# Optimization experiments

Measured on AMD Instinct MI355X. Metric: run time of the kernel, lower is better.

Reference implementation:

```python
import jax, jax.numpy as jnp
import numpy as np

B, T, C, H = 8, 1024, 1024, 16
D = C // H  # head dim = 64

def setup_inputs() -> dict:
    key = jax.random.key(0)
    k1, k2, k3 = jax.random.split(key, 3)
    x = jax.random.normal(k1, (B, T, C), dtype=jnp.float32)
    W_attn = jax.random.normal(k2, (C, 3 * C), dtype=jnp.float32) * (1.0 / np.sqrt(C))
    W_proj = jax.random.normal(k3, (C, C), dtype=jnp.float32) * (1.0 / np.sqrt(C))
    # Llama RoPE frequencies: base^(-2i/D)
    omega = (10000.0 ** (-jnp.arange(0, D, 2, dtype=jnp.float32) / D))  # [D/2]
    return {"x": x, "W_attn": W_attn, "W_proj": W_proj, "omega": omega}

def _apply_rope(x, omega):
    # x: [B, T, H, D]; omega: [D/2]
    t = x.shape[1]
    ang = jnp.arange(t, dtype=x.dtype)[:, None] * omega[None, :]  # [T, D/2]
    cos = jnp.cos(ang)[None, :, None, :]  # [1, T, 1, D/2]
    sin = jnp.sin(ang)[None, :, None, :]
    d2 = x.shape[-1] // 2
    x1, x2 = x[..., :d2], x[..., d2:]
    return jnp.concatenate([x1 * cos - x2 * sin, x2 * cos + x1 * sin], axis=-1)

def reference(x, W_attn, W_proj, omega):
    b, t, c = x.shape
    qkv = jnp.einsum('btc,cd->btd', x, W_attn)  # fused QKV projection
    q, k, v = jnp.split(qkv, 3, axis=-1)
    q = q.reshape(b, t, H, D)
    k = k.reshape(b, t, H, D)
    v = v.reshape(b, t, H, D)
    q = _apply_rope(q, omega)
    k = _apply_rope(k, omega)
    # non-causal SDPA
    scale = 1.0 / jnp.sqrt(jnp.asarray(D, dtype=x.dtype))
    scores = jnp.einsum('bqhd,bkhd->bhqk', q, k) * scale
    probs = jax.nn.softmax(scores, axis=-1)
    y = jnp.einsum('bhqk,bkhd->bqhd', probs, v).reshape(b, t, c)
    return jnp.einsum('btc,cd->btd', y, W_proj)
```

## Files before the change

### kernel.cpp

```cpp
#include <hip/hip_runtime.h>
#include <hip/hip_bf16.h>
#include <stdint.h>


typedef __attribute__((ext_vector_type(8))) short short8;
typedef __attribute__((ext_vector_type(4))) float floatx4;
typedef __attribute__((ext_vector_type(2))) unsigned int uint2v;

#define DEV static __device__ __forceinline__

#if __has_builtin(__builtin_amdgcn_exp2f)
#define EXP2(x) __builtin_amdgcn_exp2f(x)
#else
#define EXP2(x) exp2f(x)
#endif

DEV uint16_t f2bf(float f) {
  union { float f; uint32_t i; } v; v.f = f;
  uint32_t u = v.i;
  return (uint16_t)((u + 0x7fffu + ((u >> 16) & 1u)) >> 16);
}

DEV uint32_t pkbf(float a, float b) {
  __hip_bfloat162 h = __float22bfloat162_rn(make_float2(a, b));
  union { __hip_bfloat162 h; uint32_t u; } v; v.h = h;
  return v.u;
}

DEV void async_load16(const uint16_t* g, uint16_t* l) {
  __builtin_amdgcn_global_load_lds(
      (const __attribute__((address_space(1))) void*)g,
      (__attribute__((address_space(3))) void*)l, 16, 0, 0);
}

__global__ __launch_bounds__(256) void prep(
    const float* __restrict__ x, const float* __restrict__ W_attn,
    const float* __restrict__ W_proj, const float* __restrict__ omega,
    uint16_t* __restrict__ xb, uint16_t* __restrict__ Wt_attn,
    uint16_t* __restrict__ Wt_proj, float2* __restrict__ tab) {
  __shared__ uint16_t tile[64][65];
  const int blk = blockIdx.x, tid = threadIdx.x;
  if (blk < 4096) {
    const size_t base = ((size_t)blk * 256 + tid) * 8;
    floatx4 a = *(const floatx4*)(x + base);
    floatx4 b = *(const floatx4*)(x + base + 4);
    short8 s;
    s[0] = (short)f2bf(a[0]); s[1] = (short)f2bf(a[1]);
    s[2] = (short)f2bf(a[2]); s[3] = (short)f2bf(a[3]);
    s[4] = (short)f2bf(b[0]); s[5] = (short)f2bf(b[1]);
    s[6] = (short)f2bf(b[2]); s[7] = (short)f2bf(b[3]);
    *(short8*)(xb + base) = s;
  } else if (blk < 5120) {
    const float* in;
    uint16_t* out;
    int R = 1024, Ccols, bx, by;
    if (blk < 4864) {
      const int idx = blk - 4096;
      in = W_attn; out = Wt_attn; Ccols = 3072;
      bx = idx % 48; by = idx / 48;
    } else {
      const int idx = blk - 4864;
      in = W_proj; out = Wt_proj; Ccols = 1024;
      bx = idx % 16; by = idx / 16;
    }
    const int tx = tid & 63, ty = tid >> 6;
    const int c0 = bx * 64, r0 = by * 64;
    #pragma unroll
    for (int i = 0; i < 64; i += 4)
      tile[ty + i][tx] = f2bf(in[(size_t)(r0 + ty + i) * Ccols + c0 + tx]);
    __syncthreads();
    #pragma unroll
    for (int i = 0; i < 64; i += 4)
      out[(size_t)(c0 + ty + i) * R + r0 + tx] = tile[tx][ty + i];
  } else {
    const int idx = (blk - 5120) * 256 + tid;
    const int t = idx >> 5, d = idx & 31;
    float s, c;
    sincosf((float)t * omega[d], &s, &c);
    tab[idx] = make_float2(c, s);
  }
}

DEV void gemm_core8(const uint16_t* __restrict__ Ag,
                    const uint16_t* __restrict__ Bg,
                    int row0, int col0,
                    uint16_t* As, uint16_t* Bs, floatx4 (&acc)[4][4]) {
  const int tid = threadIdx.x;
  const int wave = tid >> 6, lane = tid & 63;
  const int l15 = lane & 15, quad = lane >> 4;
  const int wrow = wave >> 1, wcol = wave & 1;
  const int sw = l15 & 7;
  const int K = 1024;

  size_t aoff[4], boff[2];
  #pragma unroll
  for (int i = 0; i < 4; i++) {
    const int e = i * 512 + tid;
    const int r = e >> 3, c = e & 7, j = c ^ (r & 7);
    aoff[i] = (size_t)(row0 + r) * K + j * 8;
  }
  #pragma unroll
  for (int i = 0; i < 2; i++) {
    const int e = i * 512 + tid;
    const int r = e >> 3, c = e & 7, j = c ^ (r & 7);
    boff[i] = (size_t)(col0 + r) * K + j * 8;
  }

  #pragma unroll
  for (int t = 0; t < 2; t++) {
    #pragma unroll
    for (int i = 0; i < 2; i++)
      async_load16(Bg + boff[i] + (size_t)t * 64, Bs + t * 8192 + (i * 512 + tid) * 8);
    #pragma unroll
    for (int i = 0; i < 4; i++)
      async_load16(Ag + aoff[i] + (size_t)t * 64, As + t * 16384 + (i * 512 + tid) * 8);
  }

  const floatx4 z4 = {0.f, 0.f, 0.f, 0.f};
  #pragma unroll
  for (int mi = 0; mi < 4; mi++)
    #pragma unroll
    for (int ni = 0; ni < 4; ni++) acc[mi][ni] = z4;

  asm volatile("s_waitcnt vmcnt(6)" ::: "memory");
  __builtin_amdgcn_s_barrier();

  int qa = 0, q2 = 2;
  const int arow = wrow * 64 + l15;
  const int brow = wcol * 64 + l15;
  for (int kt = 0; kt < 16; ++kt) {
    const uint16_t* Aq = As + qa * 16384;
    const uint16_t* Bq = Bs + qa * 8192;
    uint16_t* As2 = As + q2 * 16384;
    uint16_t* Bs2 = Bs + q2 * 8192;
    const size_t k2 = (size_t)(kt + 2) * 64;

    short8 af[4], bfr[4];
    #pragma unroll
    for (int mi = 0; mi < 4; mi++)
      af[mi] = *(const short8*)(Aq + (arow + mi * 16) * 64 + ((quad ^ sw) * 8));
    #pragma unroll
    for (int ni = 0; ni < 4; ni++)
      bfr[ni] = *(const short8*)(Bq + (brow + ni * 16) * 64 + ((quad ^ sw) * 8));
    if (kt < 14) {
      #pragma unroll
      for (int i = 0; i < 2; i++)
        async_load16(Bg + boff[i] + k2, Bs2 + (i * 512 + tid) * 8);
      #pragma unroll
      for (int i = 0; i < 2; i++)
        async_load16(Ag + aoff[i] + k2, As2 + (i * 512 + tid) * 8);
    }
    __builtin_amdgcn_s_barrier();
    asm volatile("s_waitcnt lgkmcnt(0)" ::: "memory");
    __builtin_amdgcn_s_setprio(1);
    #pragma unroll
    for (int mi = 0; mi < 4; mi++)
      #pragma unroll
      for (int ni = 0; ni < 4; ni++)
        acc[mi][ni] = __builtin_amdgcn_mfma_f32_16x16x32_bf16(
            af[mi], bfr[ni], acc[mi][ni], 0, 0, 0);
    __builtin_amdgcn_s_setprio(0);
    __builtin_amdgcn_s_barrier();

    #pragma unroll
    for (int mi = 0; mi < 4; mi++)
      af[mi] = *(const short8*)(Aq + (arow + mi * 16) * 64 + (((4 + quad) ^ sw) * 8));
    #pragma unroll
    for (int ni = 0; ni < 4; ni++)
      bfr[ni] = *(const short8*)(Bq + (brow + ni * 16) * 64 + (((4 + quad) ^ sw) * 8));
    if (kt < 14) {
      #pragma unroll
      for (int i = 2; i < 4; i++)
        async_load16(Ag + aoff[i] + k2, As2 + (i * 512 + tid) * 8);
      asm volatile("s_waitcnt vmcnt(6)" ::: "memory");
    } else if (kt == 14) {
      asm volatile("s_waitcnt vmcnt(0)" ::: "memory");
    }
    __builtin_amdgcn_s_barrier();
    asm volatile("s_waitcnt lgkmcnt(0)" ::: "memory");
    __builtin_amdgcn_s_setprio(1);
    #pragma unroll
    for (int mi = 0; mi < 4; mi++)
      #pragma unroll
      for (int ni = 0; ni < 4; ni++)
        acc[mi][ni] = __builtin_amdgcn_mfma_f32_16x16x32_bf16(
            af[mi], bfr[ni], acc[mi][ni], 0, 0, 0);
    __builtin_amdgcn_s_setprio(0);
    __builtin_amdgcn_s_barrier();

    qa = (qa == 2) ? 0 : qa + 1;
    q2 = (q2 == 2) ? 0 : q2 + 1;
  }
}

__global__ __launch_bounds__(512) void gemm_qkv(
    const uint16_t* __restrict__ A, const uint16_t* __restrict__ Bt,
    const float2* __restrict__ tab,
    uint16_t* __restrict__ Qr, uint16_t* __restrict__ Kr, uint16_t* __restrict__ Vt) {
  __shared__ __align__(16) uint16_t As[3 * 256 * 64];
  __shared__ __align__(16) uint16_t Bs[3 * 128 * 64];
  const int row0 = blockIdx.y * 256, col0 = blockIdx.x * 128;
  floatx4 acc[4][4];
  gemm_core8(A, Bt, row0, col0, As, Bs, acc);

  const int tid = threadIdx.x;
  const int wave = tid >> 6, lane = tid & 63;
  const int l15 = lane & 15, quad = lane >> 4;
  const int cblk = col0 + (wave & 1) * 64;
  const int region = cblk >> 10;
  const int h = (cblk & 1023) >> 6;
  const int rr = row0 + (wave >> 1) * 64;
  const int b = rr >> 10;
  const int tbase = rr & 1023;
  const size_t bh = (size_t)b * 16 + h;

  if (region < 2) {
    uint16_t* dst = (region == 0) ? Qr : Kr;
    const float scl = (region == 0) ? 0.125f * 1.44269504088896f : 1.0f;
    #pragma unroll
    for (int mi = 0; mi < 4; mi++)
      #pragma unroll
      for (int r = 0; r < 4; r++) {
        const int t = tbase + mi * 16 + quad * 4 + r;
        const size_t base = (bh * 1024 + t) * 64;
        const float2 cs0 = tab[t * 32 + l15];
        const float2 cs1 = tab[t * 32 + l15 + 16];
        {
          float x1 = acc[mi][0][r], x2 = acc[mi][2][r];
          dst[base + l15]      = f2bf((x1 * cs0.x - x2 * cs0.y) * scl);
          dst[base + l15 + 32] = f2bf((x2 * cs0.x + x1 * cs0.y) * scl);
        }
        {
          float x1 = acc[mi][1][r], x2 = acc[mi][3][r];
          dst[base + 16 + l15]      = f2bf((x1 * cs1.x - x2 * cs1.y) * scl);
          dst[base + 16 + l15 + 32] = f2bf((x2 * cs1.x + x1 * cs1.y) * scl);
        }
      }
  } else {
    #pragma unroll
    for (int mi = 0; mi < 4; mi++)
      #pragma unroll
      for (int ni = 0; ni < 4; ni++) {
        const int d = ni * 16 + l15;
        #pragma unroll
        for (int r = 0; r < 4; r++) {
          const int t = tbase + mi * 16 + quad * 4 + r;
          Vt[bh * 65536 + (size_t)d * 1024 + t] = f2bf(acc[mi][ni][r]);
        }
      }
  }
}

__global__ __launch_bounds__(512) void gemm_out(
    const uint16_t* __restrict__ A, const uint16_t* __restrict__ Bt,
    float* __restrict__ Cmat, int M, int N, int K) {
  __shared__ __align__(16) uint16_t As[3 * 256 * 64];
  __shared__ __align__(16) uint16_t Bs[3 * 128 * 64];
  const int row0 = blockIdx.y * 256, col0 = blockIdx.x * 128;
  floatx4 acc[4][4];
  gemm_core8(A, Bt, row0, col0, As, Bs, acc);

  const int tid = threadIdx.x;
  const int wave = tid >> 6, lane = tid & 63;
  const int l15 = lane & 15, quad = lane >> 4;
  #pragma unroll
  for (int mi = 0; mi < 4; mi++)
    #pragma unroll
    for (int ni = 0; ni < 4; ni++) {
      const int col = col0 + (wave & 1) * 64 + ni * 16 + l15;
      #pragma unroll
      for (int r = 0; r < 4; r++) {
        const int row = row0 + (wave >> 1) * 64 + mi * 16 + quad * 4 + r;
        Cmat[(size_t)row * N + col] = acc[mi][ni][r];
      }
    }
}

#define FLD 72

__global__ __launch_bounds__(256) void flash_attn(
    const uint16_t* __restrict__ Qr, const uint16_t* __restrict__ Kr,
    const uint16_t* __restrict__ Vt, uint16_t* __restrict__ Y) {
  __shared__ uint16_t Ks[64 * 64];
  __shared__ uint16_t Vs[64 * 64];
  __shared__ uint16_t Ps[128 * FLD];
  const int tid = threadIdx.x;
  const int wv = tid >> 6, lane = tid & 63;
  const int l15 = lane & 15, quad = lane >> 4;
  const int sw = l15 & 7;
  const int bh = blockIdx.x & 127, qt = blockIdx.x >> 7;
  const int b = bh >> 4, h = bh & 15;
  const int q0 = qt * 128;
  const uint16_t* Qbh = Qr + (size_t)bh * 1024 * 64;
  const uint16_t* Kbh = Kr + (size_t)bh * 1024 * 64;
  const uint16_t* Vbh = Vt + (size_t)bh * 64 * 1024;

  short8 bq[2][2];
  #pragma unroll
  for (int g = 0; g < 2; g++)
    #pragma unroll
    for (int ks = 0; ks < 2; ks++)
      bq[g][ks] = *(const short8*)(Qbh +
          (size_t)(q0 + wv * 32 + g * 16 + l15) * 64 + ks * 32 + quad * 8);

  float psum[2] = {0.f, 0.f};
  const floatx4 z4 = {0.f, 0.f, 0.f, 0.f};
  floatx4 oacc[2][4];
  #pragma unroll
  for (int g = 0; g < 2; g++)
    #pragma unroll
    for (int mi = 0; mi < 4; mi++) oacc[g][mi] = z4;

  for (int kt = 0; kt < 16; kt++) {
    __syncthreads();
    #pragma unroll
    for (int i = 0; i < 2; i++) {
      const int e = i * 256 + tid;
      const int r = e >> 3;
      const int j = (e & 7) ^ (r & 7);
      async_load16(Kbh + (size_t)(kt * 64 + r) * 64 + j * 8, Ks + e * 8);
      async_load16(Vbh + (size_t)r * 1024 + kt * 64 + j * 8, Vs + e * 8);
    }
    __syncthreads();

    #pragma unroll
    for (int g = 0; g < 2; g++) {
      const int qrow = wv * 32 + g * 16 + l15;
      floatx4 sacc[4];
      #pragma unroll
      for (int ni = 0; ni < 4; ni++) {
        sacc[ni] = z4;
        #pragma unroll
        for (int ks = 0; ks < 2; ks++) {
          short8 ak = *(const short8*)(&Ks[(ni * 16 + l15) * 64 +
                                           (((ks * 4 + quad) ^ sw) * 8)]);
          sacc[ni] = __builtin_amdgcn_mfma_f32_16x16x32_bf16(ak, bq[g][ks], sacc[ni], 0, 0, 0);
        }
      }
      #pragma unroll
      for (int ni = 0; ni < 4; ni++) {
        float p0 = EXP2(sacc[ni][0]), p1 = EXP2(sacc[ni][1]);
        float p2 = EXP2(sacc[ni][2]), p3 = EXP2(sacc[ni][3]);
        psum[g] += (p0 + p1) + (p2 + p3);
        uint2v pk; pk[0] = pkbf(p0, p1); pk[1] = pkbf(p2, p3);
        *(uint2v*)(&Ps[qrow * FLD + ni * 16 + quad * 4]) = pk;
      }
      short8 bp[2];
      #pragma unroll
      for (int ks = 0; ks < 2; ks++)
        bp[ks] = *(const short8*)(&Ps[qrow * FLD + ks * 32 + quad * 8]);
      #pragma unroll
      for (int mi = 0; mi < 4; mi++) {
        #pragma unroll
        for (int ks = 0; ks < 2; ks++) {
          short8 av = *(const short8*)(&Vs[(mi * 16 + l15) * 64 +
                                           (((ks * 4 + quad) ^ sw) * 8)]);
          oacc[g][mi] = __builtin_amdgcn_mfma_f32_16x16x32_bf16(av, bp[ks], oacc[g][mi], 0, 0, 0);
        }
      }
    }
  }

  #pragma unroll
  for (int g = 0; g < 2; g++) {
    float l_tot = psum[g];
    l_tot += __shfl_xor(l_tot, 16, 64);
    l_tot += __shfl_xor(l_tot, 32, 64);
    const float linv = 1.0f / l_tot;
    const int t = q0 + wv * 32 + g * 16 + l15;
    #pragma unroll
    for (int mi = 0; mi < 4; mi++) {
      uint2v yk;
      yk[0] = pkbf(oacc[g][mi][0] * linv, oacc[g][mi][1] * linv);
      yk[1] = pkbf(oacc[g][mi][2] * linv, oacc[g][mi][3] * linv);
      *(uint2v*)(Y + (size_t)(b * 1024 + t) * 1024 + h * 64 + mi * 16 + quad * 4) = yk;
    }
  }
}

extern "C" void kernel_launch(void* const* d_in, const int* in_sizes, int n_in,
                              void* d_out, int out_size, void* d_ws, size_t ws_size,
                              hipStream_t stream) {
  const float* x      = (const float*)d_in[0];
  const float* W_attn = (const float*)d_in[1];
  const float* W_proj = (const float*)d_in[2];
  const float* omega  = (const float*)d_in[3];
  float* out = (float*)d_out;

  uint16_t* wsp     = (uint16_t*)d_ws;
  uint16_t* xb      = wsp;
  uint16_t* Wt_attn = xb + (size_t)8192 * 1024;
  uint16_t* Wt_proj = Wt_attn + (size_t)3072 * 1024;
  uint16_t* Qr      = Wt_proj + (size_t)1024 * 1024;
  uint16_t* Kr      = Qr + (size_t)128 * 1024 * 64;
  uint16_t* Vt      = Kr + (size_t)128 * 1024 * 64;
  float2*   ropet   = (float2*)(Vt + (size_t)128 * 1024 * 64);
  uint16_t* Y       = xb;

  prep<<<5248, 256, 0, stream>>>(x, W_attn, W_proj, omega, xb, Wt_attn, Wt_proj, ropet);
  gemm_qkv<<<dim3(24, 32), 512, 0, stream>>>(xb, Wt_attn, ropet, Qr, Kr, Vt);
  flash_attn<<<1024, 256, 0, stream>>>(Qr, Kr, Vt, Y);
  gemm_out<<<dim3(8, 32), 512, 0, stream>>>(Y, Wt_proj, out, 8192, 1024, 1024);
}
```

Baseline: 243.7 us.

## Use 256x256 QKV GEMM tiles and XCD-aware block mapping for both GEMMs

New measurement: 243.9 us. Within noise of the previous version (+0.1%).

```diff
diff --git a/kernel.cpp b/kernel.cpp
--- a/kernel.cpp
+++ b/kernel.cpp
@@ -81,135 +81,99 @@
   }
 }
 
-DEV void gemm_core8(const uint16_t* __restrict__ Ag,
-                    const uint16_t* __restrict__ Bg,
-                    int row0, int col0,
-                    uint16_t* As, uint16_t* Bs, floatx4 (&acc)[4][4]) {
+__global__ __launch_bounds__(512) void gemm_qkv(
+    const uint16_t* __restrict__ A, const uint16_t* __restrict__ Bt,
+    const float2* __restrict__ tab,
+    uint16_t* __restrict__ Qr, uint16_t* __restrict__ Kr, uint16_t* __restrict__ Vt) {
+  __shared__ __align__(16) uint16_t As[3 * 256 * 32];
+  __shared__ __align__(16) uint16_t Bs[3 * 256 * 32];
   const int tid = threadIdx.x;
   const int wave = tid >> 6, lane = tid & 63;
   const int l15 = lane & 15, quad = lane >> 4;
-  const int wrow = wave >> 1, wcol = wave & 1;
-  const int sw = l15 & 7;
+  const int wrow = wave >> 2, wcol = wave & 3;
+  const int sw2 = (l15 >> 1) & 3;
   const int K = 1024;
 
-  size_t aoff[4], boff[2];
-  #pragma unroll
-  for (int i = 0; i < 4; i++) {
-    const int e = i * 512 + tid;
-    const int r = e >> 3, c = e & 7, j = c ^ (r & 7);
-    aoff[i] = (size_t)(row0 + r) * K + j * 8;
-  }
+  const int bid = blockIdx.x;
+  const int xcd = bid & 7, slot = bid >> 3;
+  const int row0 = (xcd * 4 + (slot & 3)) * 256;
+  const int col0 = (slot >> 2) * 256;
+
+  size_t aoff[2], boff[2];
   #pragma unroll
   for (int i = 0; i < 2; i++) {
     const int e = i * 512 + tid;
-    const int r = e >> 3, c = e & 7, j = c ^ (r & 7);
+    const int r = e >> 2, c = e & 3;
+    const int j = c ^ ((r >> 1) & 3);
+    aoff[i] = (size_t)(row0 + r) * K + j * 8;
     boff[i] = (size_t)(col0 + r) * K + j * 8;
   }
-
-  #pragma unroll
-  for (int t = 0; t < 2; t++) {
-    #pragma unroll
-    for (int i = 0; i < 2; i++)
-      async_load16(Bg + boff[i] + (size_t)t * 64, Bs + t * 8192 + (i * 512 + tid) * 8);
-    #pragma unroll
-    for (int i = 0; i < 4; i++)
-      async_load16(Ag + aoff[i] + (size_t)t * 64, As + t * 16384 + (i * 512 + tid) * 8);
-  }
-
+  #pragma unroll
+  for (int t = 0; t < 2; t++)
+    #pragma unroll
+    for (int i = 0; i < 2; i++) {
+      async_load16(A + aoff[i] + (size_t)t * 32, As + t * 8192 + (i * 512 + tid) * 8);
+      async_load16(Bt + boff[i] + (size_t)t * 32, Bs + t * 8192 + (i * 512 + tid) * 8);
+    }
+
+  floatx4 acc[8][4];
   const floatx4 z4 = {0.f, 0.f, 0.f, 0.f};
   #pragma unroll
-  for (int mi = 0; mi < 4; mi++)
+  for (int mi = 0; mi < 8; mi++)
     #pragma unroll
     for (int ni = 0; ni < 4; ni++) acc[mi][ni] = z4;
 
-  asm volatile("s_waitcnt vmcnt(6)" ::: "memory");
+  asm volatile("s_waitcnt vmcnt(4)" ::: "memory");
   __builtin_amdgcn_s_barrier();
 
   int qa = 0, q2 = 2;
-  const int arow = wrow * 64 + l15;
+  const int arow = wrow * 128 + l15;
   const int brow = wcol * 64 + l15;
-  for (int kt = 0; kt < 16; ++kt) {
-    const uint16_t* Aq = As + qa * 16384;
+  for (int kt = 0; kt < 32; ++kt) {
+    const uint16_t* Aq = As + qa * 8192;
     const uint16_t* Bq = Bs + qa * 8192;
-    uint16_t* As2 = As + q2 * 16384;
+    uint16_t* As2 = As + q2 * 8192;
     uint16_t* Bs2 = Bs + q2 * 8192;
-    const size_t k2 = (size_t)(kt + 2) * 64;
-
-    short8 af[4], bfr[4];
-    #pragma unroll
-    for (int mi = 0; mi < 4; mi++)
-      af[mi] = *(const short8*)(Aq + (arow + mi * 16) * 64 + ((quad ^ sw) * 8));
+
+    short8 af[8], bfr[4];
+    #pragma unroll
+    for (int mi = 0; mi < 8; mi++)
+      af[mi] = *(const short8*)(Aq + (arow + mi * 16) * 32 + ((quad ^ sw2) * 8));
     #pragma unroll
     for (int ni = 0; ni < 4; ni++)
-      bfr[ni] = *(const short8*)(Bq + (brow + ni * 16) * 64 + ((quad ^ sw) * 8));
-    if (kt < 14) {
-      #pragma unroll
-      for (int i = 0; i < 2; i++)
-        async_load16(Bg + boff[i] + k2, Bs2 + (i * 512 + tid) * 8);
-      #pragma unroll
-      for (int i = 0; i < 2; i++)
-        async_load16(Ag + aoff[i] + k2, As2 + (i * 512 + tid) * 8);
+      bfr[ni] = *(const short8*)(Bq + (brow + ni * 16) * 32 + ((quad ^ sw2) * 8));
+    if (kt < 30) {
+      const size_t k2 = (size_t)(kt + 2) * 32;
+      #pragma unroll
+      for (int i = 0; i < 2; i++) {
+        async_load16(A + aoff[i] + k2, As2 + (i * 512 + tid) * 8);
+        async_load16(Bt + boff[i] + k2, Bs2 + (i * 512 + tid) * 8);
+      }
     }
     __builtin_amdgcn_s_barrier();
     asm volatile("s_waitcnt lgkmcnt(0)" ::: "memory");
     __builtin_amdgcn_s_setprio(1);
     #pragma unroll
-    for (int mi = 0; mi < 4; mi++)
+    for (int mi = 0; mi < 8; mi++)
       #pragma unroll
       for (int ni = 0; ni < 4; ni++)
         acc[mi][ni] = __builtin_amdgcn_mfma_f32_16x16x32_bf16(
             af[mi], bfr[ni], acc[mi][ni], 0, 0, 0);
     __builtin_amdgcn_s_setprio(0);
-    __builtin_amdgcn_s_barrier();
-
-    #pragma unroll
-    for (int mi = 0; mi < 4; mi++)
-      af[mi] = *(const short8*)(Aq + (arow + mi * 16) * 64 + (((4 + quad) ^ sw) * 8));
-    #pragma unroll
-    for (int ni = 0; ni < 4; ni++)
-      bfr[ni] = *(const short8*)(Bq + (brow + ni * 16) * 64 + (((4 + quad) ^ sw) * 8));
-    if (kt < 14) {
-      #pragma unroll
-      for (int i = 2; i < 4; i++)
-        async_load16(Ag + aoff[i] + k2, As2 + (i * 512 + tid) * 8);
-      asm volatile("s_waitcnt vmcnt(6)" ::: "memory");
-    } else if (kt == 14) {
+    if (kt < 30) {
+      asm volatile("s_waitcnt vmcnt(4)" ::: "memory");
+    } else if (kt == 30) {
       asm volatile("s_waitcnt vmcnt(0)" ::: "memory");
     }
     __builtin_amdgcn_s_barrier();
-    asm volatile("s_waitcnt lgkmcnt(0)" ::: "memory");
-    __builtin_amdgcn_s_setprio(1);
-    #pragma unroll
-    for (int mi = 0; mi < 4; mi++)
-      #pragma unroll
-      for (int ni = 0; ni < 4; ni++)
-        acc[mi][ni] = __builtin_amdgcn_mfma_f32_16x16x32_bf16(
-            af[mi], bfr[ni], acc[mi][ni], 0, 0, 0);
-    __builtin_amdgcn_s_setprio(0);
-    __builtin_amdgcn_s_barrier();
-
     qa = (qa == 2) ? 0 : qa + 1;
     q2 = (q2 == 2) ? 0 : q2 + 1;
   }
-}
-
-__global__ __launch_bounds__(512) void gemm_qkv(
-    const uint16_t* __restrict__ A, const uint16_t* __restrict__ Bt,
-    const float2* __restrict__ tab,
-    uint16_t* __restrict__ Qr, uint16_t* __restrict__ Kr, uint16_t* __restrict__ Vt) {
-  __shared__ __align__(16) uint16_t As[3 * 256 * 64];
-  __shared__ __align__(16) uint16_t Bs[3 * 128 * 64];
-  const int row0 = blockIdx.y * 256, col0 = blockIdx.x * 128;
-  floatx4 acc[4][4];
-  gemm_core8(A, Bt, row0, col0, As, Bs, acc);
-
-  const int tid = threadIdx.x;
-  const int wave = tid >> 6, lane = tid & 63;
-  const int l15 = lane & 15, quad = lane >> 4;
-  const int cblk = col0 + (wave & 1) * 64;
+
+  const int cblk = col0 + wcol * 64;
   const int region = cblk >> 10;
   const int h = (cblk & 1023) >> 6;
-  const int rr = row0 + (wave >> 1) * 64;
+  const int rr = row0 + wrow * 128;
   const int b = rr >> 10;
   const int tbase = rr & 1023;
   const size_t bh = (size_t)b * 16 + h;
@@ -218,7 +182,7 @@
     uint16_t* dst = (region == 0) ? Qr : Kr;
     const float scl = (region == 0) ? 0.125f * 1.44269504088896f : 1.0f;
     #pragma unroll
-    for (int mi = 0; mi < 4; mi++)
+    for (int mi = 0; mi < 8; mi++)
       #pragma unroll
       for (int r = 0; r < 4; r++) {
         const int t = tbase + mi * 16 + quad * 4 + r;
@@ -238,7 +202,7 @@
       }
   } else {
     #pragma unroll
-    for (int mi = 0; mi < 4; mi++)
+    for (int mi = 0; mi < 8; mi++)
       #pragma unroll
       for (int ni = 0; ni < 4; ni++) {
         const int d = ni * 16 + l15;
@@ -251,12 +215,127 @@
   }
 }
 
+DEV void gemm_core8(const uint16_t* __restrict__ Ag,
+                    const uint16_t* __restrict__ Bg,
+                    int row0, int col0,
+                    uint16_t* As, uint16_t* Bs, floatx4 (&acc)[4][4]) {
+  const int tid = threadIdx.x;
+  const int wave = tid >> 6, lane = tid & 63;
+  const int l15 = lane & 15, quad = lane >> 4;
+  const int wrow = wave >> 1, wcol = wave & 1;
+  const int sw = l15 & 7;
+  const int K = 1024;
+
+  size_t aoff[4], boff[2];
+  #pragma unroll
+  for (int i = 0; i < 4; i++) {
+    const int e = i * 512 + tid;
+    const int r = e >> 3, c = e & 7, j = c ^ (r & 7);
+    aoff[i] = (size_t)(row0 + r) * K + j * 8;
+  }
+  #pragma unroll
+  for (int i = 0; i < 2; i++) {
+    const int e = i * 512 + tid;
+    const int r = e >> 3, c = e & 7, j = c ^ (r & 7);
+    boff[i] = (size_t)(col0 + r) * K + j * 8;
+  }
+
+  #pragma unroll
+  for (int t = 0; t < 2; t++) {
+    #pragma unroll
+    for (int i = 0; i < 2; i++)
+      async_load16(Bg + boff[i] + (size_t)t * 64, Bs + t * 8192 + (i * 512 + tid) * 8);
+    #pragma unroll
+    for (int i = 0; i < 4; i++)
+      async_load16(Ag + aoff[i] + (size_t)t * 64, As + t * 16384 + (i * 512 + tid) * 8);
+  }
+
+  const floatx4 z4 = {0.f, 0.f, 0.f, 0.f};
+  #pragma unroll
+  for (int mi = 0; mi < 4; mi++)
+    #pragma unroll
+    for (int ni = 0; ni < 4; ni++) acc[mi][ni] = z4;
+
+  asm volatile("s_waitcnt vmcnt(6)" ::: "memory");
+  __builtin_amdgcn_s_barrier();
+
+  int qa = 0, q2 = 2;
+  const int arow = wrow * 64 + l15;
+  const int brow = wcol * 64 + l15;
+  for (int kt = 0; kt < 16; ++kt) {
+    const uint16_t* Aq = As + qa * 16384;
+    const uint16_t* Bq = Bs + qa * 8192;
+    uint16_t* As2 = As + q2 * 16384;
+    uint16_t* Bs2 = Bs + q2 * 8192;
+    const size_t k2 = (size_t)(kt + 2) * 64;
+
+    short8 af[4], bfr[4];
+    #pragma unroll
+    for (int mi = 0; mi < 4; mi++)
+      af[mi] = *(const short8*)(Aq + (arow + mi * 16) * 64 + ((quad ^ sw) * 8));
+    #pragma unroll
+    for (int ni = 0; ni < 4; ni++)
+      bfr[ni] = *(const short8*)(Bq + (brow + ni * 16) * 64 + ((quad ^ sw) * 8));
+    if (kt < 14) {
+      #pragma unroll
+      for (int i = 0; i < 2; i++)
+        async_load16(Bg + boff[i] + k2, Bs2 + (i * 512 + tid) * 8);
+      #pragma unroll
+      for (int i = 0; i < 2; i++)
+        async_load16(Ag + aoff[i] + k2, As2 + (i * 512 + tid) * 8);
+    }
+    __builtin_amdgcn_s_barrier();
+    asm volatile("s_waitcnt lgkmcnt(0)" ::: "memory");
+    __builtin_amdgcn_s_setprio(1);
+    #pragma unroll
+    for (int mi = 0; mi < 4; mi++)
+      #pragma unroll
+      for (int ni = 0; ni < 4; ni++)
+        acc[mi][ni] = __builtin_amdgcn_mfma_f32_16x16x32_bf16(
+            af[mi], bfr[ni], acc[mi][ni], 0, 0, 0);
+    __builtin_amdgcn_s_setprio(0);
+    __builtin_amdgcn_s_barrier();
+
+    #pragma unroll
+    for (int mi = 0; mi < 4; mi++)
+      af[mi] = *(const short8*)(Aq + (arow + mi * 16) * 64 + (((4 + quad) ^ sw) * 8));
+    #pragma unroll
+    for (int ni = 0; ni < 4; ni++)
+      bfr[ni] = *(const short8*)(Bq + (brow + ni * 16) * 64 + (((4 + quad) ^ sw) * 8));
+    if (kt < 14) {
+      #pragma unroll
+      for (int i = 2; i < 4; i++)
+        async_load16(Ag + aoff[i] + k2, As2 + (i * 512 + tid) * 8);
+      asm volatile("s_waitcnt vmcnt(6)" ::: "memory");
+    } else if (kt == 14) {
+      asm volatile("s_waitcnt vmcnt(0)" ::: "memory");
+    }
+    __builtin_amdgcn_s_barrier();
+    asm volatile("s_waitcnt lgkmcnt(0)" ::: "memory");
+    __builtin_amdgcn_s_setprio(1);
+    #pragma unroll
+    for (int mi = 0; mi < 4; mi++)
+      #pragma unroll
+      for (int ni = 0; ni < 4; ni++)
+        acc[mi][ni] = __builtin_amdgcn_mfma_f32_16x16x32_bf16(
+            af[mi], bfr[ni], acc[mi][ni], 0, 0, 0);
+    __builtin_amdgcn_s_setprio(0);
+    __builtin_amdgcn_s_barrier();
+
+    qa = (qa == 2) ? 0 : qa + 1;
+    q2 = (q2 == 2) ? 0 : q2 + 1;
+  }
+}
+
 __global__ __launch_bounds__(512) void gemm_out(
     const uint16_t* __restrict__ A, const uint16_t* __restrict__ Bt,
     float* __restrict__ Cmat, int M, int N, int K) {
   __shared__ __align__(16) uint16_t As[3 * 256 * 64];
   __shared__ __align__(16) uint16_t Bs[3 * 128 * 64];
-  const int row0 = blockIdx.y * 256, col0 = blockIdx.x * 128;
+  const int bid = blockIdx.x;
+  const int xcd = bid & 7, slot = bid >> 3;
+  const int row0 = (xcd * 4 + (slot & 3)) * 256;
+  const int col0 = (slot >> 2) * 128;
   floatx4 acc[4][4];
   gemm_core8(A, Bt, row0, col0, As, Bs, acc);
 
@@ -398,7 +477,7 @@
   uint16_t* Y       = xb;
 
   prep<<<5248, 256, 0, stream>>>(x, W_attn, W_proj, omega, xb, Wt_attn, Wt_proj, ropet);
-  gemm_qkv<<<dim3(24, 32), 512, 0, stream>>>(xb, Wt_attn, ropet, Qr, Kr, Vt);
+  gemm_qkv<<<384, 512, 0, stream>>>(xb, Wt_attn, ropet, Qr, Kr, Vt);
   flash_attn<<<1024, 256, 0, stream>>>(Qr, Kr, Vt, Y);
-  gemm_out<<<dim3(8, 32), 512, 0, stream>>>(Y, Wt_proj, out, 8192, 1024, 1024);
-}
+  gemm_out<<<256, 512, 0, stream>>>(Y, Wt_proj, out, 8192, 1024, 1024);
+}
```

## Double-buffer K/V tiles in flash attention and remap gemm_out blocks per XCD

Applied to the files above, without the earlier changes.

Result: no change. 244.0 us (+0.1%).

```diff
diff --git a/kernel.cpp b/kernel.cpp
--- a/kernel.cpp
+++ b/kernel.cpp
@@ -256,7 +256,10 @@
     float* __restrict__ Cmat, int M, int N, int K) {
   __shared__ __align__(16) uint16_t As[3 * 256 * 64];
   __shared__ __align__(16) uint16_t Bs[3 * 128 * 64];
-  const int row0 = blockIdx.y * 256, col0 = blockIdx.x * 128;
+  const int bid = blockIdx.x;
+  const int xcd = bid & 7, slot = bid >> 3;
+  const int row0 = (xcd * 4 + (slot & 3)) * 256;
+  const int col0 = (slot >> 2) * 128;
   floatx4 acc[4][4];
   gemm_core8(A, Bt, row0, col0, As, Bs, acc);
 
@@ -281,9 +284,9 @@
 __global__ __launch_bounds__(256) void flash_attn(
     const uint16_t* __restrict__ Qr, const uint16_t* __restrict__ Kr,
     const uint16_t* __restrict__ Vt, uint16_t* __restrict__ Y) {
-  __shared__ uint16_t Ks[64 * 64];
-  __shared__ uint16_t Vs[64 * 64];
-  __shared__ uint16_t Ps[128 * FLD];
+  __shared__ __align__(16) uint16_t Ks[2][64 * 64];
+  __shared__ __align__(16) uint16_t Vs[2][64 * 64];
+  __shared__ __align__(16) uint16_t Ps[128 * FLD];
   const int tid = threadIdx.x;
   const int wv = tid >> 6, lane = tid & 63;
   const int l15 = lane & 15, quad = lane >> 4;
@@ -291,9 +294,9 @@
   const int bh = blockIdx.x & 127, qt = blockIdx.x >> 7;
   const int b = bh >> 4, h = bh & 15;
   const int q0 = qt * 128;
-  const uint16_t* Qbh = Qr + (size_t)bh * 1024 * 64;
-  const uint16_t* Kbh = Kr + (size_t)bh * 1024 * 64;
-  const uint16_t* Vbh = Vt + (size_t)bh * 64 * 1024;
+  const uint16_t* Qbh = Qr + (size_t)bh * 65536;
+  const uint16_t* Kbh = Kr + (size_t)bh * 65536;
+  const uint16_t* Vbh = Vt + (size_t)bh * 65536;
 
   short8 bq[2][2];
   #pragma unroll
@@ -311,32 +314,39 @@
     #pragma unroll
     for (int mi = 0; mi < 4; mi++) oacc[g][mi] = z4;
 
+  #define STAGE_KV(kt_, Kd_, Vd_)                                               \
+    _Pragma("unroll")                                                           \
+    for (int i = 0; i < 2; i++) {                                               \
+      const int e = i * 256 + tid;                                              \
+      const int r = e >> 3;                                                     \
+      const int j = (e & 7) ^ (r & 7);                                          \
+      async_load16(Kbh + (size_t)((kt_) * 64 + r) * 64 + j * 8, (Kd_) + e * 8); \
+      async_load16(Vbh + (size_t)r * 1024 + (kt_) * 64 + j * 8, (Vd_) + e * 8); \
+    }
+
+  STAGE_KV(0, Ks[0], Vs[0]);
+  STAGE_KV(1, Ks[1], Vs[1]);
+  asm volatile("s_waitcnt vmcnt(4)" ::: "memory");
+  __builtin_amdgcn_s_barrier();
+
   for (int kt = 0; kt < 16; kt++) {
-    __syncthreads();
-    #pragma unroll
-    for (int i = 0; i < 2; i++) {
-      const int e = i * 256 + tid;
-      const int r = e >> 3;
-      const int j = (e & 7) ^ (r & 7);
-      async_load16(Kbh + (size_t)(kt * 64 + r) * 64 + j * 8, Ks + e * 8);
-      async_load16(Vbh + (size_t)r * 1024 + kt * 64 + j * 8, Vs + e * 8);
-    }
-    __syncthreads();
-
+    const int buf = kt & 1;
     #pragma unroll
     for (int g = 0; g < 2; g++) {
       const int qrow = wv * 32 + g * 16 + l15;
       floatx4 sacc[4];
+      __builtin_amdgcn_s_setprio(1);
       #pragma unroll
       for (int ni = 0; ni < 4; ni++) {
         sacc[ni] = z4;
         #pragma unroll
         for (int ks = 0; ks < 2; ks++) {
-          short8 ak = *(const short8*)(&Ks[(ni * 16 + l15) * 64 +
-                                           (((ks * 4 + quad) ^ sw) * 8)]);
+          short8 ak = *(const short8*)(&Ks[buf][(ni * 16 + l15) * 64 +
+                                               (((ks * 4 + quad) ^ sw) * 8)]);
           sacc[ni] = __builtin_amdgcn_mfma_f32_16x16x32_bf16(ak, bq[g][ks], sacc[ni], 0, 0, 0);
         }
       }
+      __builtin_amdgcn_s_setprio(0);
       #pragma unroll
       for (int ni = 0; ni < 4; ni++) {
         float p0 = EXP2(sacc[ni][0]), p1 = EXP2(sacc[ni][1]);
@@ -349,17 +359,27 @@
       #pragma unroll
       for (int ks = 0; ks < 2; ks++)
         bp[ks] = *(const short8*)(&Ps[qrow * FLD + ks * 32 + quad * 8]);
+      __builtin_amdgcn_s_setprio(1);
       #pragma unroll
       for (int mi = 0; mi < 4; mi++) {
         #pragma unroll
         for (int ks = 0; ks < 2; ks++) {
-          short8 av = *(const short8*)(&Vs[(mi * 16 + l15) * 64 +
-                                           (((ks * 4 + quad) ^ sw) * 8)]);
+          short8 av = *(const short8*)(&Vs[buf][(mi * 16 + l15) * 64 +
+                                               (((ks * 4 + quad) ^ sw) * 8)]);
           oacc[g][mi] = __builtin_amdgcn_mfma_f32_16x16x32_bf16(av, bp[ks], oacc[g][mi], 0, 0, 0);
         }
       }
-    }
-  }
+      __builtin_amdgcn_s_setprio(0);
+    }
+    __builtin_amdgcn_s_barrier();
+    if (kt + 2 < 16) { STAGE_KV(kt + 2, Ks[buf], Vs[buf]); }
+    if (kt + 1 < 16) {
+      if (kt + 2 < 16) asm volatile("s_waitcnt vmcnt(4)" ::: "memory");
+      else             asm volatile("s_waitcnt vmcnt(0)" ::: "memory");
+      __builtin_amdgcn_s_barrier();
+    }
+  }
+  #undef STAGE_KV
 
   #pragma unroll
   for (int g = 0; g < 2; g++) {
@@ -400,5 +420,5 @@
   prep<<<5248, 256, 0, stream>>>(x, W_attn, W_proj, omega, xb, Wt_attn, Wt_proj, ropet);
   gemm_qkv<<<dim3(24, 32), 512, 0, stream>>>(xb, Wt_attn, ropet, Qr, Kr, Vt);
   flash_attn<<<1024, 256, 0, stream>>>(Qr, Kr, Vt, Y);
-  gemm_out<<<dim3(8, 32), 512, 0, stream>>>(Y, Wt_proj, out, 8192, 1024, 1024);
-}
+  gemm_out<<<256, 512, 0, stream>>>(Y, Wt_proj, out, 8192, 1024, 1024);
+}
```
